# Kernel optimization log

Hardware: AMD Instinct MI355X
Metric: run time of the kernel (lower is better)

## Reference

```python
import jax, jax.numpy as jnp
import numpy as np

LOG2 = 0.6931471824645996  # float32 log(2), shifted-softplus offset

def ssp(v):
    return jax.nn.softplus(v) - LOG2

def setup_inputs() -> dict:
    key = jax.random.key(0)
    ks = jax.random.split(key, 8)
    B, A, N = 4, 512, 128
    n_in = n_factors = n_out = 256
    s_in = 1.0 / np.sqrt(n_in)
    s_f = 1.0 / np.sqrt(n_factors)
    return {
        "x": jax.random.normal(ks[0], (B, A, n_in), dtype=jnp.float32),
        "r_ij": jax.random.uniform(ks[1], (B, A, N), dtype=jnp.float32) * 5.0,
        "pairwise_mask": jnp.ones((B, A, N), dtype=jnp.float32),
        "in2f_w": jax.random.normal(ks[2], (n_in, n_factors), dtype=jnp.float32) * s_in,
        "in2f_b": jnp.zeros((n_factors,), dtype=jnp.float32),
        "f2out_w": jax.random.normal(ks[3], (n_factors, n_out), dtype=jnp.float32) * s_f,
        "f2out_b": jnp.zeros((n_out,), dtype=jnp.float32),
        "fw1": jax.random.normal(ks[4], (1, n_factors), dtype=jnp.float32),
        "fb1": jnp.zeros((n_factors,), dtype=jnp.float32),
        "fw2": jax.random.normal(ks[5], (n_factors, n_factors), dtype=jnp.float32) * s_f,
        "fb2": jnp.zeros((n_factors,), dtype=jnp.float32),
        "neighbors": jax.random.randint(ks[6], (B, A, N), 0, A, dtype=jnp.int64),
    }

def reference(x, r_ij, pairwise_mask, in2f_w, in2f_b, f2out_w, f2out_b,
              fw1, fb1, fw2, fb2, neighbors):
    # f_ij = r_ij.unsqueeze(-1); filter network: Dense+ssp -> Dense
    f_ij = r_ij[..., None]                                  # [B,A,N,1]
    W = ssp(f_ij @ fw1 + fb1) @ fw2 + fb2                   # [B,A,N,F]
    facts = x @ in2f_w + in2f_b                             # [B,A,F]
    B, A, N = neighbors.shape
    F = facts.shape[-1]
    # gather neighbor features along atom axis
    idx = neighbors.reshape(B, A * N)[..., None]            # [B,A*N,1]
    xj = jnp.take_along_axis(facts, idx, axis=1).reshape(B, A, N, F)
    xi = facts[:, :, None, :]                               # [B,A,1,F]
    y = xi * W * xj                                         # [B,A,N,F]
    y = ssp(y @ f2out_w + f2out_b)                          # [B,A,N,n_out]
    return y
```

## Files before the change

kernel.cpp:

```cpp
#include <hip/hip_runtime.h>
#include <hip/hip_bf16.h>
#include <stdint.h>

typedef unsigned short u16;

#define Adim 512
#define Ndim 128
#define Fdim 256
#define BA 2048

#define HS 264
#define XS 264

#define GRID 512
#define ITEMS 8

typedef __attribute__((ext_vector_type(8))) __bf16 bf16x8;
typedef __attribute__((ext_vector_type(4))) float f32x4;

union pack8 { bf16x8 v; u16 u[8]; };
union pack4 { uint2 q; u16 u[4]; };

__device__ __forceinline__ float bf2f(u16 u){
  uint32_t v = ((uint32_t)u) << 16;
  return __builtin_bit_cast(float, v);
}
__device__ __forceinline__ u16 f2bf(float f){
  uint32_t v = __builtin_bit_cast(uint32_t, f);
  v += 0x7fffu + ((v >> 16) & 1u);
  return (u16)(v >> 16);
}
__device__ __forceinline__ float ssp_f(float v){
  float m = fmaxf(v, 0.f);
  float e = __expf(-fabsf(v));
  return m + __logf(1.f + e) - 0.69314718f;
}

__global__ __launch_bounds__(256) void prep_kernel(
    const float* __restrict__ s0, u16* __restrict__ d0,
    const float* __restrict__ s1, u16* __restrict__ d1,
    const float* __restrict__ s2, u16* __restrict__ d2)
{
  __shared__ float tile[32][33];
  const float* src = (blockIdx.y == 0) ? s0 : (blockIdx.y == 1 ? s1 : s2);
  u16* dst = (blockIdx.y == 0) ? d0 : (blockIdx.y == 1 ? d1 : d2);
  int bx = (blockIdx.x & 7) * 32, by = (int)(blockIdx.x >> 3) * 32;
  int tx = threadIdx.x & 31, ty = threadIdx.x >> 5;
  #pragma unroll
  for (int r = 0; r < 4; r++)
    tile[ty + r*8][tx] = src[(size_t)(by + ty + r*8)*Fdim + bx + tx];
  __syncthreads();
  #pragma unroll
  for (int r = 0; r < 4; r++)
    dst[(size_t)(bx + ty + r*8)*Fdim + by + tx] = f2bf(tile[tx][ty + r*8]);
}

__global__ __launch_bounds__(256, 2) void facts_kernel(
    const float* __restrict__ x, const u16* __restrict__ wT,
    const float* __restrict__ bias, u16* __restrict__ facts)
{
  __shared__ __align__(16) u16 Xs[64*HS];
  const int tid = threadIdx.x;
  const int row0 = blockIdx.x * 64;

  #pragma unroll
  for (int i = 0; i < 16; i++){
    int id = i*256 + tid;
    int r = id >> 6, c4 = id & 63;
    float4 v = *(const float4*)(x + (size_t)(row0 + r)*Fdim + c4*4);
    pack4 p;
    p.u[0] = f2bf(v.x); p.u[1] = f2bf(v.y); p.u[2] = f2bf(v.z); p.u[3] = f2bf(v.w);
    *(uint2*)(Xs + r*HS + c4*4) = p.q;
  }
  __syncthreads();

  const int lane = tid & 63, wid = tid >> 6;
  const int wcol = wid * 64;
  const int l16 = lane & 15, quad = lane >> 4;

  f32x4 acc[4][4];
  #pragma unroll
  for (int mt = 0; mt < 4; mt++)
    #pragma unroll
    for (int ct = 0; ct < 4; ct++)
      acc[mt][ct] = (f32x4){0.f,0.f,0.f,0.f};

  const u16* wbase = wT + (size_t)(wcol + l16)*Fdim + quad*8;
  bf16x8 bb[2][4];
  #pragma unroll
  for (int ct = 0; ct < 4; ct++) bb[0][ct] = *(const bf16x8*)(wbase + ct*16*Fdim);

  for (int kk = 0; kk < 8; kk++){
    if (kk < 7){
      #pragma unroll
      for (int ct = 0; ct < 4; ct++)
        bb[(kk+1)&1][ct] = *(const bf16x8*)(wbase + ct*16*Fdim + (kk+1)*32);
    }
    bf16x8 af[4];
    #pragma unroll
    for (int mt = 0; mt < 4; mt++)
      af[mt] = *(const bf16x8*)(Xs + (mt*16 + l16)*HS + kk*32 + quad*8);
    #pragma unroll
    for (int mt = 0; mt < 4; mt++)
      #pragma unroll
      for (int ct = 0; ct < 4; ct++)
        acc[mt][ct] = __builtin_amdgcn_mfma_f32_16x16x32_bf16(af[mt], bb[kk&1][ct], acc[mt][ct], 0, 0, 0);
  }

  #pragma unroll
  for (int ct = 0; ct < 4; ct++){
    int f = wcol + ct*16 + l16;
    float bv = bias[f];
    #pragma unroll
    for (int mt = 0; mt < 4; mt++)
      #pragma unroll
      for (int i = 0; i < 4; i++){
        int m = mt*16 + quad*4 + i;
        facts[(size_t)(row0 + m)*Fdim + f] = f2bf(acc[mt][ct][i] + bv);
      }
  }
}

__global__ __launch_bounds__(512, 2) void fused_kernel(
    const float* __restrict__ r_ij, const u16* __restrict__ facts,
    const u16* __restrict__ fw2T, const u16* __restrict__ f2outT,
    const float* __restrict__ fw1, const float* __restrict__ fb1,
    const float* __restrict__ fb2, const float* __restrict__ f2out_b,
    const int* __restrict__ neighbors, float* __restrict__ out)
{
  __shared__ __align__(16) u16 Hs[64*HS];
  __shared__ __align__(16) u16 XJ[64*XS];
  __shared__ int   nb_s[64];
  __shared__ float r_s[64];

  const int tid  = threadIdx.x;
  const int lane = tid & 63, wid = tid >> 6;
  const int l16  = lane & 15, quad = lane >> 4;
  const int wcol = wid * 32;
  const int g    = tid & 31;
  const int rsub = tid >> 5;

  float fw1v[8], fb1v[8];
  *(float4*)(fw1v)   = *(const float4*)(fw1 + g*8);
  *(float4*)(fw1v+4) = *(const float4*)(fw1 + g*8 + 4);
  *(float4*)(fb1v)   = *(const float4*)(fb1 + g*8);
  *(float4*)(fb1v+4) = *(const float4*)(fb1 + g*8 + 4);
  float fb2v[2], obv[2];
  #pragma unroll
  for (int ct = 0; ct < 2; ct++){
    int f = wcol + ct*16 + l16;
    fb2v[ct] = fb2[f];
    obv[ct]  = f2out_b[f];
  }

  const u16* w1base = fw2T   + (size_t)(wcol + l16)*Fdim + quad*8;
  const u16* w2base = f2outT + (size_t)(wcol + l16)*Fdim + quad*8;

  f32x4 acc[4][2];
  #pragma unroll
  for (int mt = 0; mt < 4; mt++)
    #pragma unroll
    for (int ct = 0; ct < 2; ct++)
      acc[mt][ct] = (f32x4){0.f,0.f,0.f,0.f};

  bf16x8 bw[8][2];

  for (int l = 0; l < ITEMS; l++){
    const int item = l*GRID + blockIdx.x;
    const int pair = item >> 1;
    const int half = item & 1;
    const int bbase = (pair >> 9) << 9;

    if (tid < 64){
      nb_s[tid] = neighbors[(size_t)pair*Ndim + half*64 + tid];
      r_s[tid]  = r_ij[(size_t)pair*Ndim + half*64 + tid];
    }
    __syncthreads();

    #pragma unroll
    for (int kk = 0; kk < 8; kk++)
      #pragma unroll
      for (int ct = 0; ct < 2; ct++)
        bw[kk][ct] = *(const bf16x8*)(w1base + ct*16*Fdim + kk*32);

    float4 gx[4];
    #pragma unroll
    for (int i = 0; i < 4; i++){
      int row = i*16 + rsub;
      gx[i] = *(const float4*)(facts + ((size_t)(bbase + nb_s[row]))*Fdim + g*8);
    }

    #pragma unroll
    for (int i = 0; i < 4; i++){
      int row = i*16 + rsub;
      float rv = r_s[row];
      pack8 p;
      #pragma unroll
      for (int j = 0; j < 8; j++)
        p.u[j] = f2bf(ssp_f(fmaf(rv, fw1v[j], fb1v[j])));
      *(bf16x8*)(Hs + row*HS + g*8) = p.v;
    }

    #pragma unroll
    for (int i = 0; i < 4; i++){
      int row = i*16 + rsub;
      *(float4*)(XJ + row*XS + g*8) = gx[i];
    }
    __syncthreads();

    #pragma unroll
    for (int kk = 0; kk < 8; kk++){
      bf16x8 af[4];
      #pragma unroll
      for (int mt = 0; mt < 4; mt++)
        af[mt] = *(const bf16x8*)(Hs + (mt*16 + l16)*HS + kk*32 + quad*8);
      #pragma unroll
      for (int mt = 0; mt < 4; mt++)
        #pragma unroll
        for (int ct = 0; ct < 2; ct++)
          acc[mt][ct] = __builtin_amdgcn_mfma_f32_16x16x32_bf16(af[mt], bw[kk][ct], acc[mt][ct], 0, 0, 0);
    }
    __syncthreads();

    #pragma unroll
    for (int kk = 0; kk < 8; kk++)
      #pragma unroll
      for (int ct = 0; ct < 2; ct++)
        bw[kk][ct] = *(const bf16x8*)(w2base + ct*16*Fdim + kk*32);

    #pragma unroll
    for (int ct = 0; ct < 2; ct++){
      int f = wcol + ct*16 + l16;
      float xif = bf2f(facts[(size_t)pair*Fdim + f]);
      #pragma unroll
      for (int mt = 0; mt < 4; mt++){
        #pragma unroll
        for (int i = 0; i < 4; i++){
          int m = mt*16 + quad*4 + i;
          float wv = acc[mt][ct][i] + fb2v[ct];
          float y  = xif * wv * bf2f(XJ[m*XS + f]);
          Hs[m*HS + f] = f2bf(y);
          acc[mt][ct][i] = 0.f;
        }
      }
    }
    __syncthreads();

    #pragma unroll
    for (int kk = 0; kk < 8; kk++){
      bf16x8 af[4];
      #pragma unroll
      for (int mt = 0; mt < 4; mt++)
        af[mt] = *(const bf16x8*)(Hs + (mt*16 + l16)*HS + kk*32 + quad*8);
      #pragma unroll
      for (int mt = 0; mt < 4; mt++)
        #pragma unroll
        for (int ct = 0; ct < 2; ct++)
          acc[mt][ct] = __builtin_amdgcn_mfma_f32_16x16x32_bf16(af[mt], bw[kk][ct], acc[mt][ct], 0, 0, 0);
    }

    size_t obase = ((size_t)pair * Ndim + half*64) * Fdim;
    #pragma unroll
    for (int ct = 0; ct < 2; ct++){
      int f = wcol + ct*16 + l16;
      #pragma unroll
      for (int mt = 0; mt < 4; mt++){
        #pragma unroll
        for (int i = 0; i < 4; i++){
          int m = mt*16 + quad*4 + i;
          __builtin_nontemporal_store(ssp_f(acc[mt][ct][i] + obv[ct]),
                                      out + obase + (size_t)m*Fdim + f);
          acc[mt][ct][i] = 0.f;
        }
      }
    }
  }
}

extern "C" void kernel_launch(void* const* d_in, const int* in_sizes, int n_in,
                              void* d_out, int out_size, void* d_ws, size_t ws_size,
                              hipStream_t stream)
{
  const float* x        = (const float*)d_in[0];
  const float* r_ij     = (const float*)d_in[1];
  const float* in2f_w   = (const float*)d_in[3];
  const float* in2f_b   = (const float*)d_in[4];
  const float* f2out_w  = (const float*)d_in[5];
  const float* f2out_b  = (const float*)d_in[6];
  const float* fw1      = (const float*)d_in[7];
  const float* fb1      = (const float*)d_in[8];
  const float* fw2      = (const float*)d_in[9];
  const float* fb2      = (const float*)d_in[10];
  const int*   neighbors= (const int*)d_in[11];
  float* out = (float*)d_out;

  u16* facts  = (u16*)d_ws;
  u16* in2fT  = (u16*)((char*)d_ws + (1u<<20));
  u16* fw2T   = (u16*)((char*)d_ws + (1u<<20) + 1*(1u<<17));
  u16* f2outT = (u16*)((char*)d_ws + (1u<<20) + 2*(1u<<17));

  prep_kernel<<<dim3(64, 3), 256, 0, stream>>>(in2f_w, in2fT, fw2, fw2T, f2out_w, f2outT);
  facts_kernel<<<32, 256, 0, stream>>>(x, in2fT, in2f_b, facts);
  fused_kernel<<<GRID, 512, 0, stream>>>(r_ij, facts, fw2T, f2outT,
                                         fw1, fb1, fb2, f2out_b, neighbors, out);
}
```

Baseline: 444.8 us.

## Split fused kernel into 32-row quarter tiles with streamed weight chunks

Each work item now covers a quarter of a pair's neighbours (32 rows), using 256-thread blocks and twice as many blocks. Each wave computes a 32x64 output tile instead of 64x32. Weight fragments are loaded in four K-chunks, separated by sched barriers, rather than holding all eight K-steps in registers. The aim is lower register pressure and better occupancy and latency hiding. In exchange, each block rereads weights from cache for half as many rows, which doubles weight traffic per output row.

```diff
diff --git a/kernel.cpp b/kernel.cpp
--- a/kernel.cpp
+++ b/kernel.cpp
@@ -12,7 +12,8 @@
 #define HS 264
 #define XS 264
 
-#define GRID 512
+#define QR 32
+#define GRID 1024
 #define ITEMS 8
 
 typedef __attribute__((ext_vector_type(8))) __bf16 bf16x8;
@@ -121,22 +122,22 @@
   }
 }
 
-__global__ __launch_bounds__(512, 2) void fused_kernel(
+__global__ __launch_bounds__(256, 2) void fused_kernel(
     const float* __restrict__ r_ij, const u16* __restrict__ facts,
     const u16* __restrict__ fw2T, const u16* __restrict__ f2outT,
     const float* __restrict__ fw1, const float* __restrict__ fb1,
     const float* __restrict__ fb2, const float* __restrict__ f2out_b,
     const int* __restrict__ neighbors, float* __restrict__ out)
 {
-  __shared__ __align__(16) u16 Hs[64*HS];
-  __shared__ __align__(16) u16 XJ[64*XS];
-  __shared__ int   nb_s[64];
-  __shared__ float r_s[64];
+  __shared__ __align__(16) u16 Hs[QR*HS];
+  __shared__ __align__(16) u16 XJ[QR*XS];
+  __shared__ int   nb_s[QR];
+  __shared__ float r_s[QR];
 
   const int tid  = threadIdx.x;
   const int lane = tid & 63, wid = tid >> 6;
   const int l16  = lane & 15, quad = lane >> 4;
-  const int wcol = wid * 32;
+  const int wcol = wid * 64;
   const int g    = tid & 31;
   const int rsub = tid >> 5;
 
@@ -145,9 +146,9 @@
   *(float4*)(fw1v+4) = *(const float4*)(fw1 + g*8 + 4);
   *(float4*)(fb1v)   = *(const float4*)(fb1 + g*8);
   *(float4*)(fb1v+4) = *(const float4*)(fb1 + g*8 + 4);
-  float fb2v[2], obv[2];
-  #pragma unroll
-  for (int ct = 0; ct < 2; ct++){
+  float fb2v[4], obv[4];
+  #pragma unroll
+  for (int ct = 0; ct < 4; ct++){
     int f = wcol + ct*16 + l16;
     fb2v[ct] = fb2[f];
     obv[ct]  = f2out_b[f];
@@ -156,43 +157,48 @@
   const u16* w1base = fw2T   + (size_t)(wcol + l16)*Fdim + quad*8;
   const u16* w2base = f2outT + (size_t)(wcol + l16)*Fdim + quad*8;
 
-  f32x4 acc[4][2];
-  #pragma unroll
-  for (int mt = 0; mt < 4; mt++)
-    #pragma unroll
-    for (int ct = 0; ct < 2; ct++)
+  f32x4 acc[2][4];
+  #pragma unroll
+  for (int mt = 0; mt < 2; mt++)
+    #pragma unroll
+    for (int ct = 0; ct < 4; ct++)
       acc[mt][ct] = (f32x4){0.f,0.f,0.f,0.f};
 
-  bf16x8 bw[8][2];
+  bf16x8 bw[2][4];
 
   for (int l = 0; l < ITEMS; l++){
-    const int item = l*GRID + blockIdx.x;
-    const int pair = item >> 1;
-    const int half = item & 1;
+    const int q    = l*GRID + blockIdx.x;
+    const int pair = q >> 2;
+    const int qr   = q & 3;
     const int bbase = (pair >> 9) << 9;
 
-    if (tid < 64){
-      nb_s[tid] = neighbors[(size_t)pair*Ndim + half*64 + tid];
-      r_s[tid]  = r_ij[(size_t)pair*Ndim + half*64 + tid];
+    if (tid < QR){
+      nb_s[tid] = neighbors[(size_t)pair*Ndim + qr*QR + tid];
+      r_s[tid]  = r_ij[(size_t)pair*Ndim + qr*QR + tid];
     }
     __syncthreads();
 
     #pragma unroll
-    for (int kk = 0; kk < 8; kk++)
-      #pragma unroll
-      for (int ct = 0; ct < 2; ct++)
+    for (int kk = 0; kk < 2; kk++)
+      #pragma unroll
+      for (int ct = 0; ct < 4; ct++)
         bw[kk][ct] = *(const bf16x8*)(w1base + ct*16*Fdim + kk*32);
 
     float4 gx[4];
     #pragma unroll
     for (int i = 0; i < 4; i++){
-      int row = i*16 + rsub;
+      int row = i*8 + rsub;
       gx[i] = *(const float4*)(facts + ((size_t)(bbase + nb_s[row]))*Fdim + g*8);
     }
 
+    float xif[4];
+    #pragma unroll
+    for (int ct = 0; ct < 4; ct++)
+      xif[ct] = bf2f(facts[(size_t)pair*Fdim + wcol + ct*16 + l16]);
+
     #pragma unroll
     for (int i = 0; i < 4; i++){
-      int row = i*16 + rsub;
+      int row = i*8 + rsub;
       float rv = r_s[row];
       pack8 p;
       #pragma unroll
@@ -203,42 +209,52 @@
 
     #pragma unroll
     for (int i = 0; i < 4; i++){
-      int row = i*16 + rsub;
+      int row = i*8 + rsub;
       *(float4*)(XJ + row*XS + g*8) = gx[i];
     }
     __syncthreads();
 
     #pragma unroll
-    for (int kk = 0; kk < 8; kk++){
-      bf16x8 af[4];
-      #pragma unroll
-      for (int mt = 0; mt < 4; mt++)
-        af[mt] = *(const bf16x8*)(Hs + (mt*16 + l16)*HS + kk*32 + quad*8);
-      #pragma unroll
-      for (int mt = 0; mt < 4; mt++)
-        #pragma unroll
-        for (int ct = 0; ct < 2; ct++)
-          acc[mt][ct] = __builtin_amdgcn_mfma_f32_16x16x32_bf16(af[mt], bw[kk][ct], acc[mt][ct], 0, 0, 0);
+    for (int qk = 0; qk < 4; qk++){
+      if (qk > 0){
+        __builtin_amdgcn_sched_barrier(0);
+        #pragma unroll
+        for (int kk = 0; kk < 2; kk++)
+          #pragma unroll
+          for (int ct = 0; ct < 4; ct++)
+            bw[kk][ct] = *(const bf16x8*)(w1base + ct*16*Fdim + (qk*2+kk)*32);
+      }
+      #pragma unroll
+      for (int kk = 0; kk < 2; kk++){
+        bf16x8 af[2];
+        #pragma unroll
+        for (int mt = 0; mt < 2; mt++)
+          af[mt] = *(const bf16x8*)(Hs + (mt*16 + l16)*HS + (qk*2+kk)*32 + quad*8);
+        #pragma unroll
+        for (int mt = 0; mt < 2; mt++)
+          #pragma unroll
+          for (int ct = 0; ct < 4; ct++)
+            acc[mt][ct] = __builtin_amdgcn_mfma_f32_16x16x32_bf16(af[mt], bw[kk][ct], acc[mt][ct], 0, 0, 0);
+      }
     }
     __syncthreads();
 
     #pragma unroll
-    for (int kk = 0; kk < 8; kk++)
-      #pragma unroll
-      for (int ct = 0; ct < 2; ct++)
+    for (int kk = 0; kk < 2; kk++)
+      #pragma unroll
+      for (int ct = 0; ct < 4; ct++)
         bw[kk][ct] = *(const bf16x8*)(w2base + ct*16*Fdim + kk*32);
 
     #pragma unroll
-    for (int ct = 0; ct < 2; ct++){
+    for (int ct = 0; ct < 4; ct++){
       int f = wcol + ct*16 + l16;
-      float xif = bf2f(facts[(size_t)pair*Fdim + f]);
-      #pragma unroll
-      for (int mt = 0; mt < 4; mt++){
+      #pragma unroll
+      for (int mt = 0; mt < 2; mt++){
         #pragma unroll
         for (int i = 0; i < 4; i++){
           int m = mt*16 + quad*4 + i;
           float wv = acc[mt][ct][i] + fb2v[ct];
-          float y  = xif * wv * bf2f(XJ[m*XS + f]);
+          float y  = xif[ct] * wv * bf2f(XJ[m*XS + f]);
           Hs[m*HS + f] = f2bf(y);
           acc[mt][ct][i] = 0.f;
         }
@@ -247,24 +263,35 @@
     __syncthreads();
 
     #pragma unroll
-    for (int kk = 0; kk < 8; kk++){
-      bf16x8 af[4];
-      #pragma unroll
-      for (int mt = 0; mt < 4; mt++)
-        af[mt] = *(const bf16x8*)(Hs + (mt*16 + l16)*HS + kk*32 + quad*8);
-      #pragma unroll
-      for (int mt = 0; mt < 4; mt++)
-        #pragma unroll
-        for (int ct = 0; ct < 2; ct++)
-          acc[mt][ct] = __builtin_amdgcn_mfma_f32_16x16x32_bf16(af[mt], bw[kk][ct], acc[mt][ct], 0, 0, 0);
-    }
-
-    size_t obase = ((size_t)pair * Ndim + half*64) * Fdim;
-    #pragma unroll
-    for (int ct = 0; ct < 2; ct++){
+    for (int qk = 0; qk < 4; qk++){
+      if (qk > 0){
+        __builtin_amdgcn_sched_barrier(0);
+        #pragma unroll
+        for (int kk = 0; kk < 2; kk++)
+          #pragma unroll
+          for (int ct = 0; ct < 4; ct++)
+            bw[kk][ct] = *(const bf16x8*)(w2base + ct*16*Fdim + (qk*2+kk)*32);
+      }
+      #pragma unroll
+      for (int kk = 0; kk < 2; kk++){
+        bf16x8 af[2];
+        #pragma unroll
+        for (int mt = 0; mt < 2; mt++)
+          af[mt] = *(const bf16x8*)(Hs + (mt*16 + l16)*HS + (qk*2+kk)*32 + quad*8);
+        #pragma unroll
+        for (int mt = 0; mt < 2; mt++)
+          #pragma unroll
+          for (int ct = 0; ct < 4; ct++)
+            acc[mt][ct] = __builtin_amdgcn_mfma_f32_16x16x32_bf16(af[mt], bw[kk][ct], acc[mt][ct], 0, 0, 0);
+      }
+    }
+
+    size_t obase = ((size_t)pair * Ndim + qr*QR) * Fdim;
+    #pragma unroll
+    for (int ct = 0; ct < 4; ct++){
       int f = wcol + ct*16 + l16;
       #pragma unroll
-      for (int mt = 0; mt < 4; mt++){
+      for (int mt = 0; mt < 2; mt++){
         #pragma unroll
         for (int i = 0; i < 4; i++){
           int m = mt*16 + quad*4 + i;
@@ -301,6 +328,6 @@
 
   prep_kernel<<<dim3(64, 3), 256, 0, stream>>>(in2f_w, in2fT, fw2, fw2T, f2out_w, f2outT);
   facts_kernel<<<32, 256, 0, stream>>>(x, in2fT, in2f_b, facts);
-  fused_kernel<<<GRID, 512, 0, stream>>>(r_ij, facts, fw2T, f2outT,
+  fused_kernel<<<GRID, 256, 0, stream>>>(r_ij, facts, fw2T, f2outT,
                                          fw1, fb1, fb2, f2out_b, neighbors, out);
 }
```

New measurement: 575.2 us. 1.29x slower.
